# Kernel optimization log

Measured on AMD Instinct MI355X. Metric: run time of the kernel, lower is better.

The kernel has to match this reference:

```python
import jax, jax.numpy as jnp
import numpy as np

N = 100000
E = 3200000
IN, HID, OUT = 512, 256, 64
K = 10
ALPHA = 0.1


def setup_inputs() -> dict:
    key = jax.random.key(0)
    ks = jax.random.split(key, 8)
    x = jax.random.normal(ks[0], (N, IN), dtype=jnp.float32)
    edge_index = jax.random.randint(ks[1], (2, E), 0, N, dtype=jnp.int64)
    W1 = jax.random.normal(ks[2], (IN, HID), dtype=jnp.float32) / np.sqrt(IN)
    b1 = jnp.zeros((HID,), dtype=jnp.float32)
    W2 = jax.random.normal(ks[3], (HID, OUT), dtype=jnp.float32) / np.sqrt(HID)
    b2 = jnp.zeros((OUT,), dtype=jnp.float32)
    # PPR init: temp[k] = alpha*(1-alpha)^k, temp[K] = (1-alpha)^K
    temp = ALPHA * (1.0 - ALPHA) ** np.arange(K + 1)
    temp[-1] = (1.0 - ALPHA) ** K
    temp = jnp.asarray(temp, dtype=jnp.float32)
    return {"x": x, "edge_index": edge_index, "W1": W1, "b1": b1,
            "W2": W2, "b2": b2, "temp": temp}


def reference(x, edge_index, W1, b1, W2, b2, temp):
    n = x.shape[0]
    # MLP (dropout = identity in eval mode)
    h = jax.nn.relu(x @ W1 + b1) @ W2 + b2  # [N, OUT]

    # gcn_norm: add self-loops, edge_weight = 1, sym-normalize
    loops = jnp.arange(n, dtype=edge_index.dtype)
    row = jnp.concatenate([edge_index[0], loops])  # source (x_j)
    col = jnp.concatenate([edge_index[1], loops])  # target (aggregate into)
    w = jnp.ones(row.shape[0], dtype=h.dtype)
    deg = jax.ops.segment_sum(w, col, num_segments=n)
    dinv = jnp.where(deg > 0, jax.lax.rsqrt(deg), 0.0)
    norm = dinv[row] * w * dinv[col]  # [E+N]

    hidden = h * temp[0]

    def step(carry, gamma):
        cur, hid = carry
        msg = norm[:, None] * cur[row]                       # gather+scale
        cur = jax.ops.segment_sum(msg, col, num_segments=n)  # scatter-add
        hid = hid + gamma * cur
        return (cur, hid), None

    (_, hidden), _ = jax.lax.scan(step, (h, hidden), temp[1:])
    return hidden
```

## Files before the change

kernel.cpp:

```cpp
#include <hip/hip_runtime.h>
#include <hip/hip_bf16.h>

#define NN   100000
#define EE   3200000
#define INF  512
#define HIDF 256
#define OUTF 64
#define KSTEPS 10

typedef __attribute__((ext_vector_type(8))) short short8;
typedef __attribute__((ext_vector_type(4))) float floatx4;
typedef unsigned short ushort_t;

static __device__ inline short bf2s(__hip_bfloat16 h) {
    return __builtin_bit_cast(short, h);
}

static __device__ inline unsigned short f2bf(float f) {
    unsigned u = __float_as_uint(f);
    unsigned r = (u + 0x7FFFu + ((u >> 16) & 1u)) >> 16;
    return (unsigned short)r;
}

static __device__ inline float b2f(unsigned short u) {
    return __uint_as_float(((unsigned)u) << 16);
}


__global__ void zero_kernel(int* p, int n) {
    int i = blockIdx.x * 256 + threadIdx.x;
    if (i < n) p[i] = 0;
}

__global__ void count_kernel(const int* __restrict__ ei, int* __restrict__ counts) {
    int e = blockIdx.x * 256 + threadIdx.x;
    if (e < EE) atomicAdd(&counts[ei[EE + e]], 1);
}

__global__ void dinv_kernel(const int* __restrict__ counts, float* __restrict__ dinv) {
    int i = blockIdx.x * 256 + threadIdx.x;
    if (i < NN) dinv[i] = rsqrtf((float)(counts[i] + 1));
}

__global__ void scan1(const int* __restrict__ counts, int* __restrict__ offs,
                      int* __restrict__ partial) {
    __shared__ int s[256];
    int tid = threadIdx.x;
    int i = blockIdx.x * 256 + tid;
    int v = (i < NN) ? counts[i] : 0;
    s[tid] = v;
    __syncthreads();
    for (int d = 1; d < 256; d <<= 1) {
        int t = (tid >= d) ? s[tid - d] : 0;
        __syncthreads();
        s[tid] += t;
        __syncthreads();
    }
    if (i < NN) offs[i] = s[tid] - v;
    if (tid == 255) partial[blockIdx.x] = s[255];
}

__global__ void scan2(int* partial, int nblocks) {
    __shared__ int s[512];
    int tid = threadIdx.x;
    int v = (tid < nblocks) ? partial[tid] : 0;
    s[tid] = v;
    __syncthreads();
    for (int d = 1; d < 512; d <<= 1) {
        int t = (tid >= d) ? s[tid - d] : 0;
        __syncthreads();
        s[tid] += t;
        __syncthreads();
    }
    if (tid < nblocks) partial[tid] = s[tid] - v;
}

__global__ void scan3(int* __restrict__ offs, const int* __restrict__ partial) {
    int i = blockIdx.x * 256 + threadIdx.x;
    if (i < NN) offs[i] += partial[i >> 8];
    else if (i == NN) offs[NN] = EE;
}

__global__ void fill_kernel(const int* __restrict__ ei, const int* __restrict__ offs,
                            int* __restrict__ counts, int* __restrict__ srcIdx) {
    int e = blockIdx.x * 256 + threadIdx.x;
    if (e >= EE) return;
    int r = ei[e];
    int c = ei[EE + e];
    int old = atomicSub(&counts[c], 1);
    srcIdx[offs[c] + old - 1] = r;
}

__global__ void pack_w1(const float* __restrict__ W1, short* __restrict__ W1p) {
    int id = blockIdx.x * 256 + threadIdx.x;
    if (id >= INF * HIDF) return;
    int jj = id & 7, l = (id >> 3) & 15, q = (id >> 7) & 3, t = (id >> 9) & 15, kk = id >> 13;
    int k = kk * 32 + q * 8 + jj, n = t * 16 + l;
    W1p[id] = (short)f2bf(W1[k * HIDF + n]);
}

__global__ void pack_w2(const float* __restrict__ W2, short* __restrict__ W2p) {
    int id = blockIdx.x * 256 + threadIdx.x;
    if (id >= HIDF * OUTF) return;
    int jj = id & 7, l = (id >> 3) & 15, q = (id >> 7) & 3, t = (id >> 9) & 3, kk = id >> 11;
    int k = kk * 32 + q * 8 + jj, n = t * 16 + l;
    W2p[id] = (short)f2bf(W2[k * OUTF + n]);
}


__global__ __launch_bounds__(256) void mlp_kernel(
    const float* __restrict__ x, const short* __restrict__ W1p,
    const short* __restrict__ W2p, const float* __restrict__ b1,
    const float* __restrict__ b2, const float* __restrict__ temp,
    const float* __restrict__ dinv,
    ushort_t* __restrict__ z0, float* __restrict__ out) {

    __shared__ __align__(16) short xlds[64][136];
    __shared__ __align__(16) short hlds[64][HIDF + 8];

    int tid = threadIdx.x;
    int wave = tid >> 6, lane = tid & 63;
    int l16 = lane & 15, quad = lane >> 4;
    int brow = blockIdx.x * 64;

    const floatx4 zf = {0.f, 0.f, 0.f, 0.f};
    floatx4 acc[4][4];
#pragma unroll
    for (int mi = 0; mi < 4; mi++)
#pragma unroll
        for (int j = 0; j < 4; j++) acc[mi][j] = zf;

    for (int kc = 0; kc < 4; kc++) {
        __syncthreads();
#pragma unroll
        for (int i = 0; i < 8; i++) {
            int id = i * 256 + tid;
            int r = id >> 5;
            int c4 = id & 31;
            int row = brow + r;
            if (row > NN - 1) row = NN - 1;
            float4 f = *reinterpret_cast<const float4*>(
                x + (size_t)row * INF + kc * 128 + c4 * 4);
            uint2 u;
            u.x = (unsigned)f2bf(f.x) | ((unsigned)f2bf(f.y) << 16);
            u.y = (unsigned)f2bf(f.z) | ((unsigned)f2bf(f.w) << 16);
            *reinterpret_cast<uint2*>(&xlds[r][c4 * 4]) = u;
        }
        __syncthreads();
#pragma unroll
        for (int kk = 0; kk < 4; kk++) {
            int kg = kc * 4 + kk;
            short8 a[4];
#pragma unroll
            for (int mi = 0; mi < 4; mi++)
                a[mi] = *reinterpret_cast<const short8*>(
                    &xlds[mi * 16 + l16][kk * 32 + quad * 8]);
            short8 b[4];
#pragma unroll
            for (int j = 0; j < 4; j++) {
                int t = wave * 4 + j;
                b[j] = *reinterpret_cast<const short8*>(
                    W1p + (((size_t)(kg * 16 + t) * 64 + quad * 16 + l16) << 3));
            }
#pragma unroll
            for (int mi = 0; mi < 4; mi++)
#pragma unroll
                for (int j = 0; j < 4; j++)
                    acc[mi][j] = __builtin_amdgcn_mfma_f32_16x16x32_bf16(
                        a[mi], b[j], acc[mi][j], 0, 0, 0);
        }
    }

#pragma unroll
    for (int j = 0; j < 4; j++) {
        float bj = b1[wave * 64 + j * 16 + l16];
#pragma unroll
        for (int mi = 0; mi < 4; mi++)
#pragma unroll
            for (int r = 0; r < 4; r++) {
                float v = acc[mi][j][r] + bj;
                v = fmaxf(v, 0.f);
                hlds[mi * 16 + quad * 4 + r][wave * 64 + j * 16 + l16] = (short)f2bf(v);
            }
    }
    __syncthreads();

    floatx4 acc2[4];
#pragma unroll
    for (int j = 0; j < 4; j++) acc2[j] = zf;

#pragma unroll
    for (int kk = 0; kk < 8; kk++) {
        short8 a2 = *reinterpret_cast<const short8*>(&hlds[wave * 16 + l16][kk * 32 + quad * 8]);
#pragma unroll
        for (int j = 0; j < 4; j++) {
            short8 bb = *reinterpret_cast<const short8*>(
                W2p + (((size_t)(kk * 4 + j) * 64 + quad * 16 + l16) << 3));
            acc2[j] = __builtin_amdgcn_mfma_f32_16x16x32_bf16(a2, bb, acc2[j], 0, 0, 0);
        }
    }

    float t0 = temp[0];
#pragma unroll
    for (int j = 0; j < 4; j++) {
        float bb = b2[j * 16 + l16];
#pragma unroll
        for (int r = 0; r < 4; r++) {
            int row = brow + wave * 16 + quad * 4 + r;
            if (row < NN) {
                float v = acc2[j][r] + bb;
                size_t o = (size_t)row * 64 + j * 16 + l16;
                out[o] = t0 * v;
                z0[o] = f2bf(dinv[row] * v);
            }
        }
    }
}


#define BLO(u) __uint_as_float((u) << 16)
#define BHI(u) __uint_as_float((u) & 0xFFFF0000u)
#define ACC8(v)                      \
    do {                             \
        a0 += BLO((v).x);            \
        a1 += BHI((v).x);            \
        a2 += BLO((v).y);            \
        a3 += BHI((v).y);            \
        a4 += BLO((v).z);            \
        a5 += BHI((v).z);            \
        a6 += BLO((v).w);            \
        a7 += BHI((v).w);            \
    } while (0)

__global__ __launch_bounds__(256, 8) void prop_kernel(
    const int* __restrict__ srcIdx, const int* __restrict__ offs,
    const float* __restrict__ dinv, const ushort_t* __restrict__ z,
    ushort_t* __restrict__ zn, float* __restrict__ hid,
    const float* __restrict__ temp, int k, int write_z) {

    int node = blockIdx.x * 4 + (threadIdx.x >> 6);
    int lane = threadIdx.x & 63;
    int g = lane >> 3;
    int q = lane & 7;

    int beg = __builtin_amdgcn_readfirstlane(offs[node]);
    int end = __builtin_amdgcn_readfirstlane(offs[node + 1]);

    float a0 = 0.f, a1 = 0.f, a2 = 0.f, a3 = 0.f;
    float a4 = 0.f, a5 = 0.f, a6 = 0.f, a7 = 0.f;

    {
        uint4 v = reinterpret_cast<const uint4*>(z + ((size_t)node << 6))[q];
        if (g == 0) ACC8(v);
    }

    int e = beg;
    for (; e + 16 <= end; e += 16) {
        int s0 = srcIdx[e + g];
        int s1 = srcIdx[e + 8 + g];
        uint4 v0 = reinterpret_cast<const uint4*>(z + ((size_t)s0 << 6))[q];
        uint4 v1 = reinterpret_cast<const uint4*>(z + ((size_t)s1 << 6))[q];
        ACC8(v0);
        ACC8(v1);
    }
    for (; e < end; e += 8) {
        int ee = e + g;
        int cl = (ee < end) ? ee : (end - 1);
        int s = srcIdx[cl];
        uint4 v = reinterpret_cast<const uint4*>(z + ((size_t)s << 6))[q];
        if (ee < end) ACC8(v);
    }

#pragma unroll
    for (int m = 8; m < 64; m <<= 1) {
        a0 += __shfl_xor(a0, m);
        a1 += __shfl_xor(a1, m);
        a2 += __shfl_xor(a2, m);
        a3 += __shfl_xor(a3, m);
        a4 += __shfl_xor(a4, m);
        a5 += __shfl_xor(a5, m);
        a6 += __shfl_xor(a6, m);
        a7 += __shfl_xor(a7, m);
    }

    float dv = dinv[node];
    float tk = temp[k];
    float c0 = dv * a0, c1 = dv * a1, c2 = dv * a2, c3 = dv * a3;
    float c4 = dv * a4, c5 = dv * a5, c6 = dv * a6, c7 = dv * a7;

    if (g == 0) {
        float* hp = hid + ((size_t)node << 6) + q * 8;
        float4 h0 = *reinterpret_cast<float4*>(hp);
        float4 h1 = *reinterpret_cast<float4*>(hp + 4);
        h0.x += tk * c0; h0.y += tk * c1; h0.z += tk * c2; h0.w += tk * c3;
        h1.x += tk * c4; h1.y += tk * c5; h1.z += tk * c6; h1.w += tk * c7;
        *reinterpret_cast<float4*>(hp) = h0;
        *reinterpret_cast<float4*>(hp + 4) = h1;
        if (write_z) {
            uint4 u;
            u.x = (unsigned)f2bf(dv * c0) | ((unsigned)f2bf(dv * c1) << 16);
            u.y = (unsigned)f2bf(dv * c2) | ((unsigned)f2bf(dv * c3) << 16);
            u.z = (unsigned)f2bf(dv * c4) | ((unsigned)f2bf(dv * c5) << 16);
            u.w = (unsigned)f2bf(dv * c6) | ((unsigned)f2bf(dv * c7) << 16);
            reinterpret_cast<uint4*>(zn + ((size_t)node << 6))[q] = u;
        }
    }
}


extern "C" void kernel_launch(void* const* d_in, const int* in_sizes, int n_in,
                              void* d_out, int out_size, void* d_ws, size_t ws_size,
                              hipStream_t stream) {
    const float* x    = (const float*)d_in[0];
    const int*   ei   = (const int*)d_in[1];
    const float* W1   = (const float*)d_in[2];
    const float* b1   = (const float*)d_in[3];
    const float* W2   = (const float*)d_in[4];
    const float* b2   = (const float*)d_in[5];
    const float* temp = (const float*)d_in[6];
    float* out = (float*)d_out;

    char* p = (char*)d_ws;
    auto carve = [&](size_t bytes) -> char* {
        char* r = p;
        p += (bytes + 255) & ~(size_t)255;
        return r;
    };
    ushort_t* zA   = (ushort_t*)carve(sizeof(ushort_t) * (size_t)NN * 64);
    ushort_t* zB   = (ushort_t*)carve(sizeof(ushort_t) * (size_t)NN * 64);
    int* srcIdx    = (int*)carve(sizeof(int) * (size_t)EE);
    int* counts    = (int*)carve(sizeof(int) * NN);
    int* offs      = (int*)carve(sizeof(int) * (NN + 1));
    int* partial   = (int*)carve(sizeof(int) * 512);
    float* dinv    = (float*)carve(sizeof(float) * NN);
    short* W1p     = (short*)carve(sizeof(short) * INF * HIDF);
    short* W2p     = (short*)carve(sizeof(short) * HIDF * OUTF);

    const int NB = (NN + 255) / 256;

    zero_kernel<<<NB, 256, 0, stream>>>(counts, NN);
    pack_w1<<<(INF * HIDF + 255) / 256, 256, 0, stream>>>(W1, W1p);
    pack_w2<<<(HIDF * OUTF + 255) / 256, 256, 0, stream>>>(W2, W2p);

    count_kernel<<<EE / 256, 256, 0, stream>>>(ei, counts);
    dinv_kernel<<<NB, 256, 0, stream>>>(counts, dinv);
    scan1<<<NB, 256, 0, stream>>>(counts, offs, partial);
    scan2<<<1, 512, 0, stream>>>(partial, NB);
    scan3<<<(NN + 256) / 256, 256, 0, stream>>>(offs, partial);
    fill_kernel<<<EE / 256, 256, 0, stream>>>(ei, offs, counts, srcIdx);

    mlp_kernel<<<(NN + 63) / 64, 256, 0, stream>>>(x, W1p, W2p, b1, b2, temp, dinv, zA, out);

    ushort_t* a = zA;
    ushort_t* b = zB;
    for (int k = 1; k <= KSTEPS; k++) {
        prop_kernel<<<NN / 4, 256, 0, stream>>>(srcIdx, offs, dinv, a, b, out, temp, k,
                                                (k < KSTEPS) ? 1 : 0);
        ushort_t* t = a; a = b; b = t;
    }
}
```

Before: 1.268 ms.

## Pre-bin edges by destination region before CSR fill for locality

Replaces the single-pass CSR fill, whose atomics and scattered writes land anywhere across the 100k-node range, with a two-pass scheme. The first pass bins edges into 8 destination regions using wave ballots and writes packed (src, local dst) words into a reused buffer. The second pass fills each region separately, so the atomics and srcIdx writes stay within a smaller address window that can stay cache-resident. In exchange it adds an extra read of edge_index, a packed intermediate array and two more launches. The packing keeps 14 bits for the local destination index, which fits because a region holds 12500 nodes.

```diff
diff --git a/kernel.cpp b/kernel.cpp
--- a/kernel.cpp
+++ b/kernel.cpp
@@ -7,6 +7,14 @@
 #define HIDF 256
 #define OUTF 64
 #define KSTEPS 10
+
+#define NREG 8
+#define REGW (NN / NREG)
+#define BINB 256
+#define EPB  (EE / BINB)
+#define EPW  (EPB / 4)
+#define RND  ((EPW + 63) / 64)
+#define NCHF 256
 
 typedef __attribute__((ext_vector_type(8))) short short8;
 typedef __attribute__((ext_vector_type(4))) float floatx4;
@@ -81,14 +89,89 @@
     else if (i == NN) offs[NN] = EE;
 }
 
-__global__ void fill_kernel(const int* __restrict__ ei, const int* __restrict__ offs,
-                            int* __restrict__ counts, int* __restrict__ srcIdx) {
-    int e = blockIdx.x * 256 + threadIdx.x;
-    if (e >= EE) return;
-    int r = ei[e];
-    int c = ei[EE + e];
-    int old = atomicSub(&counts[c], 1);
-    srcIdx[offs[c] + old - 1] = r;
+__global__ void init_cur(const int* __restrict__ offs, int* __restrict__ gcur) {
+    int t = threadIdx.x;
+    if (t < NREG) gcur[t] = offs[t * REGW];
+}
+
+__global__ __launch_bounds__(256) void binx_kernel(
+    const int* __restrict__ ei, int* __restrict__ gcur,
+    unsigned* __restrict__ packed) {
+    __shared__ int scnt[4][NREG];
+    __shared__ int wb[4][NREG];
+    int tid = threadIdx.x, w = tid >> 6, lane = tid & 63;
+    int wstart = blockIdx.x * EPB + w * EPW;
+    unsigned long long lt = (lane == 63) ? 0x7FFFFFFFFFFFFFFFull
+                                         : ((1ull << lane) - 1ull);
+
+    int wcnt[NREG];
+#pragma unroll
+    for (int r = 0; r < NREG; r++) wcnt[r] = 0;
+
+    for (int it = 0; it < RND; it++) {
+        int idx = it * 64 + lane;
+        bool valid = idx < EPW;
+        int e = wstart + (valid ? idx : 0);
+        int c = ei[EE + e];
+        int rg = c / REGW;
+#pragma unroll
+        for (int r = 0; r < NREG; r++)
+            wcnt[r] += __popcll(__ballot(valid && rg == r));
+    }
+    if (lane == 0) {
+#pragma unroll
+        for (int r = 0; r < NREG; r++) scnt[w][r] = wcnt[r];
+    }
+    __syncthreads();
+    if (tid < NREG) {
+        int r = tid;
+        int t0 = scnt[0][r], t1 = scnt[1][r], t2 = scnt[2][r], t3 = scnt[3][r];
+        int base = atomicAdd(&gcur[r], t0 + t1 + t2 + t3);
+        wb[0][r] = base;
+        wb[1][r] = base + t0;
+        wb[2][r] = base + t0 + t1;
+        wb[3][r] = base + t0 + t1 + t2;
+    }
+    __syncthreads();
+
+    int rbase[NREG];
+#pragma unroll
+    for (int r = 0; r < NREG; r++) rbase[r] = wb[w][r];
+
+    for (int it = 0; it < RND; it++) {
+        int idx = it * 64 + lane;
+        bool valid = idx < EPW;
+        int e = wstart + (valid ? idx : 0);
+        int c = ei[EE + e];
+        int src = ei[e];
+        int rg = c / REGW;
+#pragma unroll
+        for (int r = 0; r < NREG; r++) {
+            unsigned long long mask = __ballot(valid && rg == r);
+            int myoff = __popcll(mask & lt);
+            if (valid && rg == r)
+                packed[rbase[r] + myoff] =
+                    ((unsigned)src << 14) | (unsigned)(c - r * REGW);
+            rbase[r] += __popcll(mask);
+        }
+    }
+}
+
+__global__ __launch_bounds__(256) void fillc_kernel(
+    const unsigned* __restrict__ packed, const int* __restrict__ offs,
+    int* __restrict__ counts, int* __restrict__ srcIdx) {
+    int b = blockIdx.x;
+    int r = b & 7, j = b >> 3;
+    int lo = offs[r * REGW];
+    int hi = offs[(r + 1) * REGW];
+    int base = r * REGW;
+    for (int i = lo + j * 256 + threadIdx.x; i < hi; i += NCHF * 256) {
+        unsigned p = packed[i];
+        int c = base + (int)(p & 16383u);
+        int src = (int)(p >> 14);
+        int old = atomicSub(&counts[c], 1);
+        srcIdx[offs[c] + old - 1] = src;
+    }
 }
 
 __global__ void pack_w1(const float* __restrict__ W1, short* __restrict__ W1p) {
@@ -335,6 +418,8 @@
     float* dinv    = (float*)carve(sizeof(float) * NN);
     short* W1p     = (short*)carve(sizeof(short) * INF * HIDF);
     short* W2p     = (short*)carve(sizeof(short) * HIDF * OUTF);
+    int* gcur      = (int*)carve(sizeof(int) * NREG);
+    unsigned* packed = (unsigned*)zB;
 
     const int NB = (NN + 255) / 256;
 
@@ -347,7 +432,10 @@
     scan1<<<NB, 256, 0, stream>>>(counts, offs, partial);
     scan2<<<1, 512, 0, stream>>>(partial, NB);
     scan3<<<(NN + 256) / 256, 256, 0, stream>>>(offs, partial);
-    fill_kernel<<<EE / 256, 256, 0, stream>>>(ei, offs, counts, srcIdx);
+
+    init_cur<<<1, 64, 0, stream>>>(offs, gcur);
+    binx_kernel<<<BINB, 256, 0, stream>>>(ei, gcur, packed);
+    fillc_kernel<<<NCHF * NREG, 256, 0, stream>>>(packed, offs, counts, srcIdx);
 
     mlp_kernel<<<(NN + 63) / 64, 256, 0, stream>>>(x, W1p, W2p, b1, b2, temp, dinv, zA, out);
 
```

After: 1.320 ms. 1.04x slower.

## Replace atomic CSR fill with two-pass radix binning and LDS-local fill

Applied to the files above, without the earlier changes.

The single fill kernel, which did a global atomicSub per edge and scattered writes across the whole srcIdx array, is replaced by a three-stage counting sort. Edges are first binned by coarse destination range (8192 nodes) using wave ballots and one atomic per block per bin, then sub-binned into 256-node buckets, and finally each bucket is placed into CSR order in shared memory and written out contiguously. The aim is to remove random global atomics and scattered writes in favour of coalesced streaming passes. The cost is extra passes over the edge data and reuse of the zA/zB buffers as scratch, plus a fixed LDS buffer size that must hold every bucket's edges.

```diff
diff --git a/kernel.cpp b/kernel.cpp
--- a/kernel.cpp
+++ b/kernel.cpp
@@ -8,9 +8,20 @@
 #define OUTF 64
 #define KSTEPS 10
 
+#define R1SH 13
+#define NR1  13
+#define B1B  256
+#define E1PB (EE / B1B)
+#define E1PW (E1PB / 4)
+#define R1ND ((E1PW + 63) / 64)
+#define NBIN 391
+#define CH2  32
+#define LBUF 12544
+
 typedef __attribute__((ext_vector_type(8))) short short8;
 typedef __attribute__((ext_vector_type(4))) float floatx4;
 typedef unsigned short ushort_t;
+typedef unsigned long long ull_t;
 
 static __device__ inline short bf2s(__hip_bfloat16 h) {
     return __builtin_bit_cast(short, h);
@@ -81,14 +92,179 @@
     else if (i == NN) offs[NN] = EE;
 }
 
-__global__ void fill_kernel(const int* __restrict__ ei, const int* __restrict__ offs,
-                            int* __restrict__ counts, int* __restrict__ srcIdx) {
-    int e = blockIdx.x * 256 + threadIdx.x;
-    if (e >= EE) return;
-    int r = ei[e];
-    int c = ei[EE + e];
-    int old = atomicSub(&counts[c], 1);
-    srcIdx[offs[c] + old - 1] = r;
+__global__ void init_cur(const int* __restrict__ offs, int* __restrict__ gcur1,
+                         int* __restrict__ gcur2) {
+    int t = blockIdx.x * 256 + threadIdx.x;
+    if (t < NR1) gcur1[t] = offs[t << R1SH];
+    if (t < NBIN) gcur2[t] = offs[t << 8];
+    else if (t < NR1 * 32) gcur2[t] = EE;
+}
+
+__global__ __launch_bounds__(256) void bin1_kernel(
+    const int* __restrict__ ei, int* __restrict__ gcur1,
+    unsigned* __restrict__ packed1) {
+    __shared__ int scnt[4][NR1];
+    __shared__ int wb[4][NR1];
+    int tid = threadIdx.x, w = tid >> 6, lane = tid & 63;
+    int wstart = blockIdx.x * E1PB + w * E1PW;
+    ull_t lt = (lane == 63) ? 0x7FFFFFFFFFFFFFFFull : ((1ull << lane) - 1ull);
+
+    int wcnt[NR1];
+#pragma unroll
+    for (int r = 0; r < NR1; r++) wcnt[r] = 0;
+
+    for (int it = 0; it < R1ND; it++) {
+        int idx = it * 64 + lane;
+        bool valid = idx < E1PW;
+        int e = wstart + (valid ? idx : 0);
+        int c = ei[EE + e];
+        int rg = c >> R1SH;
+#pragma unroll
+        for (int r = 0; r < NR1; r++)
+            wcnt[r] += __popcll(__ballot(valid && rg == r));
+    }
+    if (lane == 0) {
+#pragma unroll
+        for (int r = 0; r < NR1; r++) scnt[w][r] = wcnt[r];
+    }
+    __syncthreads();
+    if (tid < NR1) {
+        int r = tid;
+        int t0 = scnt[0][r], t1 = scnt[1][r], t2 = scnt[2][r], t3 = scnt[3][r];
+        int base = atomicAdd(&gcur1[r], t0 + t1 + t2 + t3);
+        wb[0][r] = base;
+        wb[1][r] = base + t0;
+        wb[2][r] = base + t0 + t1;
+        wb[3][r] = base + t0 + t1 + t2;
+    }
+    __syncthreads();
+
+    int rbase[NR1];
+#pragma unroll
+    for (int r = 0; r < NR1; r++) rbase[r] = wb[w][r];
+
+    for (int it = 0; it < R1ND; it++) {
+        int idx = it * 64 + lane;
+        bool valid = idx < E1PW;
+        int e = wstart + (valid ? idx : 0);
+        int c = ei[EE + e];
+        int src = ei[e];
+        int rg = c >> R1SH;
+#pragma unroll
+        for (int r = 0; r < NR1; r++) {
+            ull_t mask = __ballot(valid && rg == r);
+            if (valid && rg == r)
+                packed1[rbase[r] + __popcll(mask & lt)] =
+                    ((unsigned)src << R1SH) | (unsigned)(c & 8191);
+            rbase[r] += __popcll(mask);
+        }
+    }
+}
+
+__global__ __launch_bounds__(256) void bin2_kernel(
+    const unsigned* __restrict__ packed1, const int* __restrict__ offs,
+    int* __restrict__ gcur2, unsigned* __restrict__ packed2) {
+    __shared__ int scnt[4][32];
+    __shared__ int wb[4][32];
+    int b = blockIdx.x;
+    int r = b >> 5, j = b & 31;
+    int rn0 = r << R1SH;
+    int rn1 = rn0 + (1 << R1SH); if (rn1 > NN) rn1 = NN;
+    int rlo = offs[rn0], rhi = offs[rn1];
+    int len = rhi - rlo;
+    int per = (len + CH2 - 1) / CH2;
+    int clo = rlo + j * per;
+    int chi = clo + per; if (chi > rhi) chi = rhi;
+    if (clo > chi) clo = chi;
+
+    int tid = threadIdx.x, w = tid >> 6, lane = tid & 63;
+    int cl = chi - clo;
+    int wper = (cl + 3) >> 2;
+    int wlo = clo + w * wper;
+    int whi = wlo + wper; if (whi > chi) whi = chi;
+    if (wlo > whi) wlo = whi;
+    ull_t lt = (lane == 63) ? 0x7FFFFFFFFFFFFFFFull : ((1ull << lane) - 1ull);
+
+    int wcnt[32];
+#pragma unroll
+    for (int s = 0; s < 32; s++) wcnt[s] = 0;
+
+    for (int base = wlo; base < whi; base += 64) {
+        int idx = base + lane;
+        bool valid = idx < whi;
+        unsigned p = packed1[valid ? idx : wlo];
+        int sb = (int)((p & 8191u) >> 8);
+#pragma unroll
+        for (int s = 0; s < 32; s++)
+            wcnt[s] += __popcll(__ballot(valid && sb == s));
+    }
+    if (lane == 0) {
+#pragma unroll
+        for (int s = 0; s < 32; s++) scnt[w][s] = wcnt[s];
+    }
+    __syncthreads();
+    if (tid < 32) {
+        int s = tid;
+        int t0 = scnt[0][s], t1 = scnt[1][s], t2 = scnt[2][s], t3 = scnt[3][s];
+        int base = atomicAdd(&gcur2[r * 32 + s], t0 + t1 + t2 + t3);
+        wb[0][s] = base;
+        wb[1][s] = base + t0;
+        wb[2][s] = base + t0 + t1;
+        wb[3][s] = base + t0 + t1 + t2;
+    }
+    __syncthreads();
+
+    int rbase[32];
+#pragma unroll
+    for (int s = 0; s < 32; s++) rbase[s] = wb[w][s];
+
+    for (int base = wlo; base < whi; base += 64) {
+        int idx = base + lane;
+        bool valid = idx < whi;
+        unsigned p = packed1[valid ? idx : wlo];
+        int loc = (int)(p & 8191u);
+        int sb = loc >> 8;
+        unsigned src = p >> R1SH;
+#pragma unroll
+        for (int s = 0; s < 32; s++) {
+            ull_t mask = __ballot(valid && sb == s);
+            if (valid && sb == s)
+                packed2[rbase[s] + __popcll(mask & lt)] =
+                    (src << 8) | (unsigned)(loc & 255);
+            rbase[s] += __popcll(mask);
+        }
+    }
+}
+
+__global__ __launch_bounds__(256) void fill_lds_kernel(
+    const unsigned* __restrict__ packed2, const int* __restrict__ offs,
+    int* __restrict__ srcIdx) {
+    __shared__ int offsL[257];
+    __shared__ int cnt[256];
+    __shared__ int buf[LBUF];
+    int b = blockIdx.x;
+    int nb0 = b << 8;
+    int tid = threadIdx.x;
+    for (int t = tid; t < 257; t += 256) {
+        int node = nb0 + t;
+        if (node > NN) node = NN;
+        offsL[t] = offs[node];
+    }
+    __syncthreads();
+    int segBase = offsL[0];
+    int segEnd = offsL[256];
+    int len = segEnd - segBase;
+    cnt[tid] = offsL[tid + 1] - offsL[tid];
+    __syncthreads();
+    for (int i = segBase + tid; i < segEnd; i += 256) {
+        unsigned p = packed2[i];
+        int c = (int)(p & 255u);
+        int src = (int)(p >> 8);
+        int old = atomicSub(&cnt[c], 1);
+        buf[offsL[c] - segBase + old - 1] = src;
+    }
+    __syncthreads();
+    for (int i = tid; i < len; i += 256) srcIdx[segBase + i] = buf[i];
 }
 
 __global__ void pack_w1(const float* __restrict__ W1, short* __restrict__ W1p) {
@@ -335,6 +511,10 @@
     float* dinv    = (float*)carve(sizeof(float) * NN);
     short* W1p     = (short*)carve(sizeof(short) * INF * HIDF);
     short* W2p     = (short*)carve(sizeof(short) * HIDF * OUTF);
+    int* gcur1     = (int*)carve(sizeof(int) * NR1);
+    int* gcur2     = (int*)carve(sizeof(int) * NR1 * 32);
+    unsigned* packed1 = (unsigned*)zB;
+    unsigned* packed2 = (unsigned*)zA;
 
     const int NB = (NN + 255) / 256;
 
@@ -347,7 +527,11 @@
     scan1<<<NB, 256, 0, stream>>>(counts, offs, partial);
     scan2<<<1, 512, 0, stream>>>(partial, NB);
     scan3<<<(NN + 256) / 256, 256, 0, stream>>>(offs, partial);
-    fill_kernel<<<EE / 256, 256, 0, stream>>>(ei, offs, counts, srcIdx);
+
+    init_cur<<<2, 256, 0, stream>>>(offs, gcur1, gcur2);
+    bin1_kernel<<<B1B, 256, 0, stream>>>(ei, gcur1, packed1);
+    bin2_kernel<<<NR1 * 32, 256, 0, stream>>>(packed1, offs, gcur2, packed2);
+    fill_lds_kernel<<<NBIN, 256, 0, stream>>>(packed2, offs, srcIdx);
 
     mlp_kernel<<<(NN + 63) / 64, 256, 0, stream>>>(x, W1p, W2p, b1, b2, temp, dinv, zA, out);
 
```

Measured after the change: 1.321 ms. 4.2% more time.
